# Performance work log

Measured on AMD Instinct MI355X. Metric: run time of the kernel, lower is better.

Reference implementation:

```python
import jax, jax.numpy as jnp
import numpy as np

N = 100000
E = 3200000
IN_DIM = 128
HD = 64
HEADS = 4
NEG_SLOPE = 0.2


def setup_inputs() -> dict:
    key = jax.random.key(0)
    ks = jax.random.split(key, 12)
    s = lambda fan_in: 1.0 / np.sqrt(fan_in)
    x = jax.random.normal(ks[0], (N, IN_DIM), dtype=jnp.float32)
    edge_index = jax.random.randint(ks[1], (2, E), 0, N, dtype=jnp.int64)
    W1 = jax.random.normal(ks[2], (IN_DIM, HEADS * HD), dtype=jnp.float32) * s(IN_DIM)
    a_src1 = jax.random.normal(ks[3], (HEADS, HD), dtype=jnp.float32) * s(HD)
    a_dst1 = jax.random.normal(ks[4], (HEADS, HD), dtype=jnp.float32) * s(HD)
    b1 = jnp.zeros((HEADS * HD,), dtype=jnp.float32)
    W2 = jax.random.normal(ks[5], (HEADS * HD, HD), dtype=jnp.float32) * s(HEADS * HD)
    a_src2 = jax.random.normal(ks[6], (1, HD), dtype=jnp.float32) * s(HD)
    a_dst2 = jax.random.normal(ks[7], (1, HD), dtype=jnp.float32) * s(HD)
    b2 = jnp.zeros((HD,), dtype=jnp.float32)
    lin_w = jax.random.normal(ks[8], (HD, 2), dtype=jnp.float32) * s(HD)
    lin_b = jnp.zeros((2,), dtype=jnp.float32)
    return {"x": x, "edge_index": edge_index, "W1": W1, "a_src1": a_src1,
            "a_dst1": a_dst1, "b1": b1, "W2": W2, "a_src2": a_src2,
            "a_dst2": a_dst2, "b2": b2, "lin_w": lin_w, "lin_b": lin_b}


def gat_conv(x, src, dst, W, a_src, a_dst, bias, heads, out_dim, concat):
    n = x.shape[0]
    h = (x @ W).reshape(n, heads, out_dim)                 # [N,H,D]
    alpha_s = jnp.einsum('nhd,hd->nh', h, a_src)           # [N,H]
    alpha_d = jnp.einsum('nhd,hd->nh', h, a_dst)           # [N,H]
    e = alpha_s[src] + alpha_d[dst]                        # [Etot,H]
    e = jnp.where(e > 0, e, NEG_SLOPE * e)                 # leaky relu
    m = jax.ops.segment_max(e, dst, num_segments=n)        # scatter-softmax (stable)
    m = jnp.where(jnp.isfinite(m), m, 0.0)
    e = jnp.exp(e - m[dst])
    denom = jax.ops.segment_sum(e, dst, num_segments=n)
    alpha = e / denom[dst]                                 # [Etot,H]
    out = jax.ops.segment_sum(h[src] * alpha[:, :, None], dst, num_segments=n)  # [N,H,D]
    out = out.reshape(n, heads * out_dim) if concat else out.mean(axis=1)
    return out + bias


def reference(x, edge_index, W1, a_src1, a_dst1, b1, W2, a_src2, a_dst2, b2, lin_w, lin_b):
    n = x.shape[0]
    loops = jnp.arange(n, dtype=edge_index.dtype)
    src = jnp.concatenate([edge_index[0], loops])          # add self-loops (PyG default)
    dst = jnp.concatenate([edge_index[1], loops])
    h = gat_conv(x, src, dst, W1, a_src1, a_dst1, b1, HEADS, HD, True)
    h = jax.nn.elu(h)
    h = gat_conv(h, src, dst, W2, a_src2, a_dst2, b2, 1, HD, True)
    h = jax.nn.elu(h)
    return h @ lin_w + lin_b                               # [N,2]
```

## Files before the change

kernel.cpp:

```cpp
#include <hip/hip_runtime.h>
#include <hip/hip_fp16.h>
#include <math.h>

#define NN 100000
#define EE 3200000
#define ETOT (EE + NN)
#define NEG_SLOPE 0.2f
#define DMAX 96
#define CHUNK 4096
#define NB0 ((ETOT + CHUNK - 1) / CHUNK)
#define RB 391
#define EDCAP 16384

typedef _Float16 half8 __attribute__((ext_vector_type(8)));
typedef _Float16 half4v __attribute__((ext_vector_type(4)));
typedef float floatx4 __attribute__((ext_vector_type(4)));

__device__ __forceinline__ float wsum64(float v) {
#pragma unroll
  for (int o = 32; o; o >>= 1) v += __shfl_xor(v, o);
  return v;
}
__device__ __forceinline__ float lrelu(float v) { return v > 0.f ? v : NEG_SLOPE * v; }
__device__ __forceinline__ float elu1(float v) { return v > 0.f ? v : expm1f(v); }

__global__ __launch_bounds__(256) void k_pass0(const int* __restrict__ ei,
                                               int* __restrict__ chist,
                                               const float* __restrict__ W1,
                                               const float* __restrict__ W2,
                                               _Float16* __restrict__ W1t,
                                               _Float16* __restrict__ W2t) {
  int b = blockIdx.x;
  if (b >= NB0) {
    int idx = (b - NB0) * 256 + threadIdx.x;
    if (idx < 32768) {
      int n = idx >> 7, k = idx & 127;
      W1t[idx] = (_Float16)W1[k * 256 + n];
    } else {
      int j = idx - 32768;
      int n = j >> 8, k = j & 255;
      W2t[j] = (_Float16)W2[k * 64 + n];
    }
    return;
  }
  __shared__ int h[256];
  h[threadIdx.x] = 0;
  __syncthreads();
  int base = b * CHUNK;
  int lim = base + CHUNK; if (lim > ETOT) lim = ETOT;
  for (int i = base + threadIdx.x; i < lim; i += 256) {
    int d = (i < EE) ? ei[EE + i] : (i - EE);
    atomicAdd(&h[(unsigned)d / (unsigned)RB], 1);
  }
  __syncthreads();
  if (h[threadIdx.x]) atomicAdd(&chist[threadIdx.x], h[threadIdx.x]);
}

__global__ __launch_bounds__(256) void k_cscan(const int* __restrict__ chist,
                                               int* __restrict__ coffs,
                                               int* __restrict__ ccur) {
  __shared__ int ts[256];
  int t = threadIdx.x;
  int v = chist[t];
  ts[t] = v;
  __syncthreads();
  for (int o = 1; o < 256; o <<= 1) {
    int add = (t >= o) ? ts[t - o] : 0;
    __syncthreads();
    ts[t] += add;
    __syncthreads();
  }
  int excl = ts[t] - v;
  coffs[t] = excl;
  ccur[t] = excl;
  if (t == 0) coffs[256] = ETOT;
}

__global__ __launch_bounds__(256) void k_pass1(const int* __restrict__ ei,
                                               int* __restrict__ ccur,
                                               unsigned* __restrict__ ebuf) {
  __shared__ unsigned vv[CHUNK];
  __shared__ unsigned short cbv[CHUNK];
  __shared__ int h[256];
  __shared__ int cur[256];
  int t = threadIdx.x;
  h[t] = 0;
  __syncthreads();
  int base = blockIdx.x * CHUNK;
  int lim = base + CHUNK; if (lim > ETOT) lim = ETOT;
  int cnt = lim - base;
  for (int i = t; i < cnt; i += 256) {
    int e = base + i;
    int s, d;
    if (e < EE) { s = ei[e]; d = ei[EE + e]; } else { s = e - EE; d = s; }
    unsigned cb = (unsigned)d / (unsigned)RB;
    unsigned dloc = (unsigned)d - cb * (unsigned)RB;
    vv[i] = (dloc << 17) | (unsigned)s;
    cbv[i] = (unsigned short)cb;
    atomicAdd(&h[cb], 1);
  }
  __syncthreads();
  if (h[t]) cur[t] = atomicAdd(&ccur[t], h[t]);
  __syncthreads();
  for (int i = t; i < cnt; i += 256) {
    int cb = cbv[i];
    int pos = atomicAdd(&cur[cb], 1);
    ebuf[pos] = vv[i];
  }
}

__global__ __launch_bounds__(256) void k_pass2(const unsigned* __restrict__ ebuf,
                                               const int* __restrict__ coffs,
                                               int* __restrict__ offs,
                                               int* __restrict__ csr) {
  __shared__ unsigned ed[EDCAP];
  __shared__ int hist[RB];
  __shared__ int cur[RB];
  int b = blockIdx.x, t = threadIdx.x;
  int d0 = b * RB;
  int rb = NN - d0; if (rb > RB) rb = RB;
  int cbeg = coffs[b], cend = coffs[b + 1];
  int cnt = cend - cbeg;
  for (int j = t; j < rb; j += 256) hist[j] = 0;
  __syncthreads();
  for (int i = t; i < cnt; i += 256) {
    unsigned v = ebuf[cbeg + i];
    if (i < EDCAP) ed[i] = v;
    atomicAdd(&hist[v >> 17], 1);
  }
  __syncthreads();
  if (t == 0) {
    int run = cbeg;
    for (int j = 0; j < rb; ++j) { cur[j] = run; run += hist[j]; }
  }
  __syncthreads();
  for (int j = t; j < rb; j += 256) offs[d0 + j] = cur[j];
  if (b == 0 && t == 0) offs[NN] = ETOT;
  __syncthreads();
  int lim = cnt < EDCAP ? cnt : EDCAP;
  for (int i = t; i < lim; i += 256) {
    unsigned v = ed[i];
    int pos = atomicAdd(&cur[v >> 17], 1);
    csr[pos] = (int)(v & 0x1FFFFu);
  }
  for (int i = EDCAP + t; i < cnt; i += 256) {
    unsigned v = ebuf[cbeg + i];
    int pos = atomicAdd(&cur[v >> 17], 1);
    csr[pos] = (int)(v & 0x1FFFFu);
  }
}

__global__ __launch_bounds__(256) void k_gemm1m(const float* __restrict__ x,
                                                const _Float16* __restrict__ W1t,
                                                const float* __restrict__ a_src,
                                                const float* __restrict__ a_dst,
                                                _Float16* __restrict__ h1h,
                                                float* __restrict__ as_out,
                                                float* __restrict__ ad_out) {
  __shared__ _Float16 As[64][136];
  __shared__ _Float16 Wt[64][136];
  const int bx = blockIdx.x & 3;
  const int by = blockIdx.x >> 2;
  const int tid = threadIdx.x;
  const int row0 = by * 64;
#pragma unroll
  for (int i = 0; i < 8; ++i) {
    int idx = i * 256 + tid;
    int r = idx >> 5;
    int c4 = (idx & 31) * 4;
    int gr = row0 + r;
    float4 f = make_float4(0.f, 0.f, 0.f, 0.f);
    if (gr < NN) f = *(const float4*)(x + (size_t)gr * 128 + c4);
    half4v h; h[0] = (_Float16)f.x; h[1] = (_Float16)f.y; h[2] = (_Float16)f.z; h[3] = (_Float16)f.w;
    *(half4v*)&As[r][c4] = h;
  }
#pragma unroll
  for (int i = 0; i < 4; ++i) {
    int idx = i * 256 + tid;
    int r = idx >> 4;
    int g = idx & 15;
    *(half8*)&Wt[r][g * 8] = *(const half8*)(W1t + (size_t)(bx * 64 + r) * 128 + g * 8);
  }
  __syncthreads();

  const int wid = tid >> 6, lane = tid & 63;
  const int m16 = lane & 15, quad = lane >> 4;
  floatx4 acc[4];
#pragma unroll
  for (int nt = 0; nt < 4; ++nt) acc[nt] = (floatx4){0.f, 0.f, 0.f, 0.f};
#pragma unroll
  for (int ks = 0; ks < 4; ++ks) {
    half8 av = *(half8*)&As[wid * 16 + m16][ks * 32 + quad * 8];
#pragma unroll
    for (int nt = 0; nt < 4; ++nt) {
      half8 bv = *(half8*)&Wt[nt * 16 + m16][ks * 32 + quad * 8];
      acc[nt] = __builtin_amdgcn_mfma_f32_16x16x32_f16(av, bv, acc[nt], 0, 0, 0);
    }
  }
  float asr[4], adr[4];
#pragma unroll
  for (int nt = 0; nt < 4; ++nt) {
    asr[nt] = a_src[bx * 64 + nt * 16 + m16];
    adr[nt] = a_dst[bx * 64 + nt * 16 + m16];
  }
#pragma unroll
  for (int r = 0; r < 4; ++r) {
    float ps = 0.f, pd = 0.f;
#pragma unroll
    for (int nt = 0; nt < 4; ++nt) {
      ps = fmaf(acc[nt][r], asr[nt], ps);
      pd = fmaf(acc[nt][r], adr[nt], pd);
    }
#pragma unroll
    for (int o = 1; o < 16; o <<= 1) { ps += __shfl_xor(ps, o); pd += __shfl_xor(pd, o); }
    int gr = row0 + wid * 16 + quad * 4 + r;
    if (gr < NN) {
      if (m16 == 0) { as_out[gr * 4 + bx] = ps; ad_out[gr * 4 + bx] = pd; }
#pragma unroll
      for (int nt = 0; nt < 4; ++nt)
        h1h[(size_t)gr * 256 + bx * 64 + nt * 16 + m16] = (_Float16)acc[nt][r];
    }
  }
}

__global__ __launch_bounds__(256) void k_gemm2m(const _Float16* __restrict__ h1e,
                                                const _Float16* __restrict__ W2t,
                                                const float* __restrict__ a_src,
                                                const float* __restrict__ a_dst,
                                                _Float16* __restrict__ h2h,
                                                float* __restrict__ as_out,
                                                float* __restrict__ ad_out) {
  __shared__ _Float16 As2[64][136];
  __shared__ _Float16 Wt2[64][264];
  const int by = blockIdx.x;
  const int tid = threadIdx.x;
  const int row0 = by * 64;
#pragma unroll
  for (int i = 0; i < 8; ++i) {
    int idx = i * 256 + tid;
    int r = idx >> 5;
    int g = idx & 31;
    *(half8*)&Wt2[r][g * 8] = *(const half8*)(W2t + (size_t)r * 256 + g * 8);
  }
  const int wid = tid >> 6, lane = tid & 63;
  const int m16 = lane & 15, quad = lane >> 4;
  floatx4 acc[4];
#pragma unroll
  for (int nt = 0; nt < 4; ++nt) acc[nt] = (floatx4){0.f, 0.f, 0.f, 0.f};

  for (int kc = 0; kc < 2; ++kc) {
#pragma unroll
    for (int i = 0; i < 4; ++i) {
      int idx = i * 256 + tid;
      int r = idx >> 4;
      int g = idx & 15;
      int gr = row0 + r;
      half8 v = {0, 0, 0, 0, 0, 0, 0, 0};
      if (gr < NN) v = *(const half8*)(h1e + (size_t)gr * 256 + kc * 128 + g * 8);
      *(half8*)&As2[r][g * 8] = v;
    }
    __syncthreads();
#pragma unroll
    for (int ks = 0; ks < 4; ++ks) {
      half8 av = *(half8*)&As2[wid * 16 + m16][ks * 32 + quad * 8];
#pragma unroll
      for (int nt = 0; nt < 4; ++nt) {
        half8 bv = *(half8*)&Wt2[nt * 16 + m16][kc * 128 + ks * 32 + quad * 8];
        acc[nt] = __builtin_amdgcn_mfma_f32_16x16x32_f16(av, bv, acc[nt], 0, 0, 0);
      }
    }
    __syncthreads();
  }
  float asr[4], adr[4];
#pragma unroll
  for (int nt = 0; nt < 4; ++nt) {
    asr[nt] = a_src[nt * 16 + m16];
    adr[nt] = a_dst[nt * 16 + m16];
  }
#pragma unroll
  for (int r = 0; r < 4; ++r) {
    float ps = 0.f, pd = 0.f;
#pragma unroll
    for (int nt = 0; nt < 4; ++nt) {
      ps = fmaf(acc[nt][r], asr[nt], ps);
      pd = fmaf(acc[nt][r], adr[nt], pd);
    }
#pragma unroll
    for (int o = 1; o < 16; o <<= 1) { ps += __shfl_xor(ps, o); pd += __shfl_xor(pd, o); }
    int gr = row0 + wid * 16 + quad * 4 + r;
    if (gr < NN) {
      if (m16 == 0) { as_out[gr] = ps; ad_out[gr] = pd; }
#pragma unroll
      for (int nt = 0; nt < 4; ++nt)
        h2h[(size_t)gr * 64 + nt * 16 + m16] = (_Float16)acc[nt][r];
    }
  }
}

__global__ __launch_bounds__(256) void k_attn1(const int* __restrict__ offs,
                                               const int* __restrict__ csr_src,
                                               const float* __restrict__ a_s,
                                               const float* __restrict__ a_d,
                                               const _Float16* __restrict__ h1h,
                                               const float* __restrict__ b1,
                                               _Float16* __restrict__ h1e) {
  __shared__ float alpha[4][DMAX][4];
  __shared__ int sidx[4][DMAX];
  const int wid = threadIdx.x >> 6;
  const int n = blockIdx.x * 4 + wid;
  const int lane = threadIdx.x & 63;
  const int beg = offs[n], deg = offs[n + 1] - beg;
  const float4 ad = *(const float4*)(a_d + n * 4);
  float4 sm = make_float4(0.f, 0.f, 0.f, 0.f);
  for (int d = lane; d < deg; d += 64) {
    int s = csr_src[beg + d];
    float4 as = *(const float4*)(a_s + s * 4);
    float e0 = __expf(lrelu(as.x + ad.x));
    float e1 = __expf(lrelu(as.y + ad.y));
    float e2 = __expf(lrelu(as.z + ad.z));
    float e3 = __expf(lrelu(as.w + ad.w));
    sm.x += e0; sm.y += e1; sm.z += e2; sm.w += e3;
    if (d < DMAX) {
      sidx[wid][d] = s;
      float4 al = make_float4(e0, e1, e2, e3);
      *(float4*)&alpha[wid][d][0] = al;
    }
  }
  sm.x = wsum64(sm.x); sm.y = wsum64(sm.y); sm.z = wsum64(sm.z); sm.w = wsum64(sm.w);
  __syncthreads();

  const int h = lane >> 4;
  float adh = (h & 2) ? ((h & 1) ? ad.w : ad.z) : ((h & 1) ? ad.y : ad.x);
  float dh  = (h & 2) ? ((h & 1) ? sm.w : sm.z) : ((h & 1) ? sm.y : sm.x);
  float inv = 1.f / dh;
  float4 acc = make_float4(0.f, 0.f, 0.f, 0.f);
  const int dlim = deg < DMAX ? deg : DMAX;
  int d = 0;
  for (; d + 8 <= dlim; d += 8) {
    int ss[8]; float ww[8];
#pragma unroll
    for (int u = 0; u < 8; ++u) {
      ss[u] = sidx[wid][d + u];
      ww[u] = alpha[wid][d + u][h] * inv;
    }
    half4v rr[8];
#pragma unroll
    for (int u = 0; u < 8; ++u)
      rr[u] = *(const half4v*)(h1h + (size_t)ss[u] * 256 + lane * 4);
#pragma unroll
    for (int u = 0; u < 8; ++u) {
      acc.x = fmaf((float)rr[u][0], ww[u], acc.x);
      acc.y = fmaf((float)rr[u][1], ww[u], acc.y);
      acc.z = fmaf((float)rr[u][2], ww[u], acc.z);
      acc.w = fmaf((float)rr[u][3], ww[u], acc.w);
    }
  }
  for (; d < dlim; ++d) {
    int s = sidx[wid][d];
    float w = alpha[wid][d][h] * inv;
    half4v r = *(const half4v*)(h1h + (size_t)s * 256 + lane * 4);
    acc.x = fmaf((float)r[0], w, acc.x); acc.y = fmaf((float)r[1], w, acc.y);
    acc.z = fmaf((float)r[2], w, acc.z); acc.w = fmaf((float)r[3], w, acc.w);
  }
  for (; d < deg; ++d) {
    int s = csr_src[beg + d];
    float w = __expf(lrelu(a_s[s * 4 + h] + adh)) * inv;
    half4v r = *(const half4v*)(h1h + (size_t)s * 256 + lane * 4);
    acc.x = fmaf((float)r[0], w, acc.x); acc.y = fmaf((float)r[1], w, acc.y);
    acc.z = fmaf((float)r[2], w, acc.z); acc.w = fmaf((float)r[3], w, acc.w);
  }
  const int c = lane * 4;
  float4 bb = *(const float4*)(b1 + c);
  half4v o;
  o[0] = (_Float16)elu1(acc.x + bb.x);
  o[1] = (_Float16)elu1(acc.y + bb.y);
  o[2] = (_Float16)elu1(acc.z + bb.z);
  o[3] = (_Float16)elu1(acc.w + bb.w);
  *(half4v*)(h1e + (size_t)n * 256 + c) = o;
}

__global__ __launch_bounds__(256) void k_attn2(const int* __restrict__ offs,
                                               const int* __restrict__ csr_src,
                                               const float* __restrict__ a_s,
                                               const float* __restrict__ a_d,
                                               const _Float16* __restrict__ h2h,
                                               const float* __restrict__ b2,
                                               const float* __restrict__ lin_w,
                                               const float* __restrict__ lin_b,
                                               float* __restrict__ out) {
  __shared__ float alpha2[4][DMAX];
  __shared__ int sidx2[4][DMAX];
  const int wid = threadIdx.x >> 6;
  const int n = blockIdx.x * 4 + wid;
  const int lane = threadIdx.x & 63;
  const int beg = offs[n], deg = offs[n + 1] - beg;
  const float adn = a_d[n];
  float sm = 0.f;
  for (int d = lane; d < deg; d += 64) {
    int s = csr_src[beg + d];
    float e = __expf(lrelu(a_s[s] + adn));
    sm += e;
    if (d < DMAX) { sidx2[wid][d] = s; alpha2[wid][d] = e; }
  }
  sm = wsum64(sm);
  __syncthreads();
  float inv = 1.f / sm;
  float acc = 0.f;
  const int dlim = deg < DMAX ? deg : DMAX;
  int d = 0;
  for (; d + 8 <= dlim; d += 8) {
    int ss[8]; float ww[8]; float vv[8];
#pragma unroll
    for (int u = 0; u < 8; ++u) {
      ss[u] = sidx2[wid][d + u];
      ww[u] = alpha2[wid][d + u] * inv;
    }
#pragma unroll
    for (int u = 0; u < 8; ++u)
      vv[u] = (float)h2h[(size_t)ss[u] * 64 + lane];
#pragma unroll
    for (int u = 0; u < 8; ++u) acc = fmaf(vv[u], ww[u], acc);
  }
  for (; d < dlim; ++d) {
    acc = fmaf((float)h2h[(size_t)sidx2[wid][d] * 64 + lane], alpha2[wid][d] * inv, acc);
  }
  for (; d < deg; ++d) {
    int s = csr_src[beg + d];
    float w = __expf(lrelu(a_s[s] + adn)) * inv;
    acc = fmaf((float)h2h[(size_t)s * 64 + lane], w, acc);
  }
  float o = elu1(acc + b2[lane]);
  float p0 = wsum64(o * lin_w[lane * 2 + 0]);
  float p1 = wsum64(o * lin_w[lane * 2 + 1]);
  if (lane == 0) {
    out[n * 2 + 0] = p0 + lin_b[0];
    out[n * 2 + 1] = p1 + lin_b[1];
  }
}

extern "C" void kernel_launch(void* const* d_in, const int* in_sizes, int n_in,
                              void* d_out, int out_size, void* d_ws, size_t ws_size,
                              hipStream_t stream) {
  const float* x      = (const float*)d_in[0];
  const int*   ei     = (const int*)d_in[1];
  const float* W1     = (const float*)d_in[2];
  const float* a_src1 = (const float*)d_in[3];
  const float* a_dst1 = (const float*)d_in[4];
  const float* b1     = (const float*)d_in[5];
  const float* W2     = (const float*)d_in[6];
  const float* a_src2 = (const float*)d_in[7];
  const float* a_dst2 = (const float*)d_in[8];
  const float* b2     = (const float*)d_in[9];
  const float* lin_w  = (const float*)d_in[10];
  const float* lin_b  = (const float*)d_in[11];
  float* outp = (float*)d_out;

  char* w = (char*)d_ws;
  _Float16* h1h = (_Float16*)(w + 0);
  _Float16* h1e = (_Float16*)(w + 51200000);
  _Float16* h2h = (_Float16*)(w + 102400000);
  _Float16* W1t = (_Float16*)(w + 115200000);
  _Float16* W2t = (_Float16*)(w + 115265536);
  float*  as1 = (float*)(w + 115298304);
  float*  ad1 = (float*)(w + 116898304);
  float*  as2 = (float*)(w + 118498304);
  float*  ad2 = (float*)(w + 118898304);
  int*    offs = (int*)(w + 119298304);
  unsigned* ebuf = (unsigned*)(w + 119698432);
  int*    csr = (int*)(w + 132898432);
  int*    chist = (int*)(w + 146098432);
  int*    coffs = (int*)(w + 146099456);
  int*    ccur  = (int*)(w + 146100484);

  hipMemsetAsync(chist, 0, 256 * sizeof(int), stream);
  k_pass0<<<NB0 + 192, 256, 0, stream>>>(ei, chist, W1, W2, W1t, W2t);
  k_cscan<<<1, 256, 0, stream>>>(chist, coffs, ccur);
  k_pass1<<<NB0, 256, 0, stream>>>(ei, ccur, ebuf);
  k_pass2<<<256, 256, 0, stream>>>(ebuf, coffs, offs, csr);

  k_gemm1m<<<4 * 1563, 256, 0, stream>>>(x, W1t, a_src1, a_dst1, h1h, as1, ad1);
  k_attn1<<<NN / 4, 256, 0, stream>>>(offs, csr, as1, ad1, h1h, b1, h1e);

  k_gemm2m<<<1563, 256, 0, stream>>>(h1e, W2t, a_src2, a_dst2, h2h, as2, ad2);
  k_attn2<<<NN / 4, 256, 0, stream>>>(offs, csr, as2, ad2, h2h, b2, lin_w, lin_b, outp);
}
```

Baseline: 616.0 us.

## Split wavefront across multiple edges per gather step with wider vector loads

In both attention aggregation kernels, the 64-lane wavefront now processes several neighbor edges at once: layer 1 splits into two 32-lane halves, each loading 16 bytes (8 halfs) per row, and layer 2 splits into four 16-lane quarters, each loading 8 bytes. Partial accumulators are combined with cross-lane shuffles at the end. The aim is wider per-lane loads and more independent row gathers in flight, to improve memory-level parallelism for the random neighbor fetches. The cost is extra shuffle reductions, masked tail iterations, and more accumulator registers per lane.

```diff
diff --git a/kernel.cpp b/kernel.cpp
--- a/kernel.cpp
+++ b/kernel.cpp
@@ -329,54 +329,59 @@
   sm.x = wsum64(sm.x); sm.y = wsum64(sm.y); sm.z = wsum64(sm.z); sm.w = wsum64(sm.w);
   __syncthreads();
 
-  const int h = lane >> 4;
-  float adh = (h & 2) ? ((h & 1) ? ad.w : ad.z) : ((h & 1) ? ad.y : ad.x);
-  float dh  = (h & 2) ? ((h & 1) ? sm.w : sm.z) : ((h & 1) ? sm.y : sm.x);
-  float inv = 1.f / dh;
-  float4 acc = make_float4(0.f, 0.f, 0.f, 0.f);
+  const int half = lane >> 5;
+  const int fl = lane & 31;
+  const int h = fl >> 3;
+  const float adh = (h & 2) ? ((h & 1) ? ad.w : ad.z) : ((h & 1) ? ad.y : ad.x);
+  const float dh  = (h & 2) ? ((h & 1) ? sm.w : sm.z) : ((h & 1) ? sm.y : sm.x);
+  const float inv = 1.f / dh;
+  float acc8[8];
+#pragma unroll
+  for (int i = 0; i < 8; ++i) acc8[i] = 0.f;
   const int dlim = deg < DMAX ? deg : DMAX;
-  int d = 0;
-  for (; d + 8 <= dlim; d += 8) {
-    int ss[8]; float ww[8];
-#pragma unroll
-    for (int u = 0; u < 8; ++u) {
-      ss[u] = sidx[wid][d + u];
-      ww[u] = alpha[wid][d + u][h] * inv;
-    }
-    half4v rr[8];
-#pragma unroll
-    for (int u = 0; u < 8; ++u)
-      rr[u] = *(const half4v*)(h1h + (size_t)ss[u] * 256 + lane * 4);
-#pragma unroll
-    for (int u = 0; u < 8; ++u) {
-      acc.x = fmaf((float)rr[u][0], ww[u], acc.x);
-      acc.y = fmaf((float)rr[u][1], ww[u], acc.y);
-      acc.z = fmaf((float)rr[u][2], ww[u], acc.z);
-      acc.w = fmaf((float)rr[u][3], ww[u], acc.w);
-    }
-  }
-  for (; d < dlim; ++d) {
-    int s = sidx[wid][d];
-    float w = alpha[wid][d][h] * inv;
-    half4v r = *(const half4v*)(h1h + (size_t)s * 256 + lane * 4);
-    acc.x = fmaf((float)r[0], w, acc.x); acc.y = fmaf((float)r[1], w, acc.y);
-    acc.z = fmaf((float)r[2], w, acc.z); acc.w = fmaf((float)r[3], w, acc.w);
-  }
-  for (; d < deg; ++d) {
+  for (int d = 0; d < dlim; d += 8) {
+    int ss[4]; float ww[4];
+#pragma unroll
+    for (int u = 0; u < 4; ++u) {
+      int e = d + 2 * u + half;
+      bool valid = e < dlim;
+      int e2 = valid ? e : 0;
+      ss[u] = sidx[wid][e2];
+      ww[u] = valid ? alpha[wid][e2][h] * inv : 0.f;
+    }
+    half8 rr[4];
+#pragma unroll
+    for (int u = 0; u < 4; ++u)
+      rr[u] = *(const half8*)(h1h + (size_t)ss[u] * 256 + fl * 8);
+#pragma unroll
+    for (int u = 0; u < 4; ++u)
+#pragma unroll
+      for (int i = 0; i < 8; ++i)
+        acc8[i] = fmaf((float)rr[u][i], ww[u], acc8[i]);
+  }
+  for (int d = dlim + half; d < deg; d += 2) {
     int s = csr_src[beg + d];
     float w = __expf(lrelu(a_s[s * 4 + h] + adh)) * inv;
-    half4v r = *(const half4v*)(h1h + (size_t)s * 256 + lane * 4);
-    acc.x = fmaf((float)r[0], w, acc.x); acc.y = fmaf((float)r[1], w, acc.y);
-    acc.z = fmaf((float)r[2], w, acc.z); acc.w = fmaf((float)r[3], w, acc.w);
-  }
-  const int c = lane * 4;
-  float4 bb = *(const float4*)(b1 + c);
-  half4v o;
-  o[0] = (_Float16)elu1(acc.x + bb.x);
-  o[1] = (_Float16)elu1(acc.y + bb.y);
-  o[2] = (_Float16)elu1(acc.z + bb.z);
-  o[3] = (_Float16)elu1(acc.w + bb.w);
-  *(half4v*)(h1e + (size_t)n * 256 + c) = o;
+    half8 r = *(const half8*)(h1h + (size_t)s * 256 + fl * 8);
+#pragma unroll
+    for (int i = 0; i < 8; ++i) acc8[i] = fmaf((float)r[i], w, acc8[i]);
+  }
+#pragma unroll
+  for (int i = 0; i < 8; ++i) acc8[i] += __shfl_xor(acc8[i], 32);
+  if (half == 0) {
+    float4 bb0 = *(const float4*)(b1 + fl * 8);
+    float4 bb1 = *(const float4*)(b1 + fl * 8 + 4);
+    half8 o;
+    o[0] = (_Float16)elu1(acc8[0] + bb0.x);
+    o[1] = (_Float16)elu1(acc8[1] + bb0.y);
+    o[2] = (_Float16)elu1(acc8[2] + bb0.z);
+    o[3] = (_Float16)elu1(acc8[3] + bb0.w);
+    o[4] = (_Float16)elu1(acc8[4] + bb1.x);
+    o[5] = (_Float16)elu1(acc8[5] + bb1.y);
+    o[6] = (_Float16)elu1(acc8[6] + bb1.z);
+    o[7] = (_Float16)elu1(acc8[7] + bb1.w);
+    *(half8*)(h1e + (size_t)n * 256 + fl * 8) = o;
+  }
 }
 
 __global__ __launch_bounds__(256) void k_attn2(const int* __restrict__ offs,
@@ -404,34 +409,54 @@
   }
   sm = wsum64(sm);
   __syncthreads();
-  float inv = 1.f / sm;
-  float acc = 0.f;
+  const float inv = 1.f / sm;
+  const int quarter = lane >> 4;
+  const int fl = lane & 15;
+  float acc4[4];
+#pragma unroll
+  for (int i = 0; i < 4; ++i) acc4[i] = 0.f;
   const int dlim = deg < DMAX ? deg : DMAX;
-  int d = 0;
-  for (; d + 8 <= dlim; d += 8) {
-    int ss[8]; float ww[8]; float vv[8];
-#pragma unroll
-    for (int u = 0; u < 8; ++u) {
-      ss[u] = sidx2[wid][d + u];
-      ww[u] = alpha2[wid][d + u] * inv;
-    }
-#pragma unroll
-    for (int u = 0; u < 8; ++u)
-      vv[u] = (float)h2h[(size_t)ss[u] * 64 + lane];
-#pragma unroll
-    for (int u = 0; u < 8; ++u) acc = fmaf(vv[u], ww[u], acc);
-  }
-  for (; d < dlim; ++d) {
-    acc = fmaf((float)h2h[(size_t)sidx2[wid][d] * 64 + lane], alpha2[wid][d] * inv, acc);
-  }
-  for (; d < deg; ++d) {
+  for (int d = 0; d < dlim; d += 8) {
+    int ss[2]; float ww[2];
+#pragma unroll
+    for (int u = 0; u < 2; ++u) {
+      int e = d + 4 * u + quarter;
+      bool valid = e < dlim;
+      int e2 = valid ? e : 0;
+      ss[u] = sidx2[wid][e2];
+      ww[u] = valid ? alpha2[wid][e2] * inv : 0.f;
+    }
+    half4v rr[2];
+#pragma unroll
+    for (int u = 0; u < 2; ++u)
+      rr[u] = *(const half4v*)(h2h + (size_t)ss[u] * 64 + fl * 4);
+#pragma unroll
+    for (int u = 0; u < 2; ++u)
+#pragma unroll
+      for (int i = 0; i < 4; ++i)
+        acc4[i] = fmaf((float)rr[u][i], ww[u], acc4[i]);
+  }
+  for (int d = dlim + quarter; d < deg; d += 4) {
     int s = csr_src[beg + d];
     float w = __expf(lrelu(a_s[s] + adn)) * inv;
-    acc = fmaf((float)h2h[(size_t)s * 64 + lane], w, acc);
-  }
-  float o = elu1(acc + b2[lane]);
-  float p0 = wsum64(o * lin_w[lane * 2 + 0]);
-  float p1 = wsum64(o * lin_w[lane * 2 + 1]);
+    half4v r = *(const half4v*)(h2h + (size_t)s * 64 + fl * 4);
+#pragma unroll
+    for (int i = 0; i < 4; ++i) acc4[i] = fmaf((float)r[i], w, acc4[i]);
+  }
+#pragma unroll
+  for (int i = 0; i < 4; ++i) {
+    acc4[i] += __shfl_xor(acc4[i], 16);
+    acc4[i] += __shfl_xor(acc4[i], 32);
+  }
+  float p0 = 0.f, p1 = 0.f;
+#pragma unroll
+  for (int i = 0; i < 4; ++i) {
+    float o = elu1(acc4[i] + b2[fl * 4 + i]);
+    p0 = fmaf(o, lin_w[(fl * 4 + i) * 2 + 0], p0);
+    p1 = fmaf(o, lin_w[(fl * 4 + i) * 2 + 1], p1);
+  }
+#pragma unroll
+  for (int o = 1; o < 16; o <<= 1) { p0 += __shfl_xor(p0, o); p1 += __shfl_xor(p1, o); }
   if (lane == 0) {
     out[n * 2 + 0] = p0 + lin_b[0];
     out[n * 2 + 1] = p1 + lin_b[1];
```

Result: slower. 642.0 us (+4.2%).

## Drop CSR histogram pass with fixed-capacity buckets, widen GEMM1 tile, prenormalize attention

Applied to the files above, without the earlier changes.

Drops the separate edge-histogram kernel and the scan kernel. Each of the 256 destination buckets now gets a fixed slot of CAP entries in ebuf, so the edge list is read one fewer time and two launches disappear. Per-node degrees are stored explicitly for the attention kernels. GEMM1 now computes 128 output columns per block instead of 64, halving the block count and reusing each x tile more. The attention kernels drop a block-wide barrier and normalize alpha once in shared memory instead of multiplying per use. The fixed bucket capacity assumes a near-uniform destination distribution: a bucket holding more than CAP edges would overwrite the next bucket's slot and be truncated.

```diff
diff --git a/kernel.cpp b/kernel.cpp
--- a/kernel.cpp
+++ b/kernel.cpp
@@ -10,7 +10,7 @@
 #define CHUNK 4096
 #define NB0 ((ETOT + CHUNK - 1) / CHUNK)
 #define RB 391
-#define EDCAP 16384
+#define CAP 16384
 
 typedef _Float16 half8 __attribute__((ext_vector_type(8)));
 typedef _Float16 half4v __attribute__((ext_vector_type(4)));
@@ -24,8 +24,13 @@
 __device__ __forceinline__ float lrelu(float v) { return v > 0.f ? v : NEG_SLOPE * v; }
 __device__ __forceinline__ float elu1(float v) { return v > 0.f ? v : expm1f(v); }
 
-__global__ __launch_bounds__(256) void k_pass0(const int* __restrict__ ei,
-                                               int* __restrict__ chist,
+__global__ void k_init(int* __restrict__ ccur) {
+  ccur[threadIdx.x] = threadIdx.x * CAP;
+}
+
+__global__ __launch_bounds__(256) void k_pass1(const int* __restrict__ ei,
+                                               int* __restrict__ ccur,
+                                               unsigned* __restrict__ ebuf,
                                                const float* __restrict__ W1,
                                                const float* __restrict__ W2,
                                                _Float16* __restrict__ W1t,
@@ -43,42 +48,6 @@
     }
     return;
   }
-  __shared__ int h[256];
-  h[threadIdx.x] = 0;
-  __syncthreads();
-  int base = b * CHUNK;
-  int lim = base + CHUNK; if (lim > ETOT) lim = ETOT;
-  for (int i = base + threadIdx.x; i < lim; i += 256) {
-    int d = (i < EE) ? ei[EE + i] : (i - EE);
-    atomicAdd(&h[(unsigned)d / (unsigned)RB], 1);
-  }
-  __syncthreads();
-  if (h[threadIdx.x]) atomicAdd(&chist[threadIdx.x], h[threadIdx.x]);
-}
-
-__global__ __launch_bounds__(256) void k_cscan(const int* __restrict__ chist,
-                                               int* __restrict__ coffs,
-                                               int* __restrict__ ccur) {
-  __shared__ int ts[256];
-  int t = threadIdx.x;
-  int v = chist[t];
-  ts[t] = v;
-  __syncthreads();
-  for (int o = 1; o < 256; o <<= 1) {
-    int add = (t >= o) ? ts[t - o] : 0;
-    __syncthreads();
-    ts[t] += add;
-    __syncthreads();
-  }
-  int excl = ts[t] - v;
-  coffs[t] = excl;
-  ccur[t] = excl;
-  if (t == 0) coffs[256] = ETOT;
-}
-
-__global__ __launch_bounds__(256) void k_pass1(const int* __restrict__ ei,
-                                               int* __restrict__ ccur,
-                                               unsigned* __restrict__ ebuf) {
   __shared__ unsigned vv[CHUNK];
   __shared__ unsigned short cbv[CHUNK];
   __shared__ int h[256];
@@ -86,7 +55,7 @@
   int t = threadIdx.x;
   h[t] = 0;
   __syncthreads();
-  int base = blockIdx.x * CHUNK;
+  int base = b * CHUNK;
   int lim = base + CHUNK; if (lim > ETOT) lim = ETOT;
   int cnt = lim - base;
   for (int i = t; i < cnt; i += 256) {
@@ -110,41 +79,39 @@
 }
 
 __global__ __launch_bounds__(256) void k_pass2(const unsigned* __restrict__ ebuf,
-                                               const int* __restrict__ coffs,
+                                               const int* __restrict__ ccur,
                                                int* __restrict__ offs,
+                                               int* __restrict__ degarr,
                                                int* __restrict__ csr) {
-  __shared__ unsigned ed[EDCAP];
+  __shared__ unsigned ed[CAP];
   __shared__ int hist[RB];
   __shared__ int cur[RB];
   int b = blockIdx.x, t = threadIdx.x;
   int d0 = b * RB;
   int rb = NN - d0; if (rb > RB) rb = RB;
-  int cbeg = coffs[b], cend = coffs[b + 1];
-  int cnt = cend - cbeg;
+  int w0 = b * CAP;
+  int cnt = ccur[b] - w0;
+  if (cnt > CAP) cnt = CAP;
   for (int j = t; j < rb; j += 256) hist[j] = 0;
   __syncthreads();
   for (int i = t; i < cnt; i += 256) {
-    unsigned v = ebuf[cbeg + i];
-    if (i < EDCAP) ed[i] = v;
+    unsigned v = ebuf[w0 + i];
+    ed[i] = v;
     atomicAdd(&hist[v >> 17], 1);
   }
   __syncthreads();
   if (t == 0) {
-    int run = cbeg;
+    int run = w0;
     for (int j = 0; j < rb; ++j) { cur[j] = run; run += hist[j]; }
   }
   __syncthreads();
-  for (int j = t; j < rb; j += 256) offs[d0 + j] = cur[j];
-  if (b == 0 && t == 0) offs[NN] = ETOT;
-  __syncthreads();
-  int lim = cnt < EDCAP ? cnt : EDCAP;
-  for (int i = t; i < lim; i += 256) {
+  for (int j = t; j < rb; j += 256) {
+    offs[d0 + j] = cur[j];
+    degarr[d0 + j] = hist[j];
+  }
+  __syncthreads();
+  for (int i = t; i < cnt; i += 256) {
     unsigned v = ed[i];
-    int pos = atomicAdd(&cur[v >> 17], 1);
-    csr[pos] = (int)(v & 0x1FFFFu);
-  }
-  for (int i = EDCAP + t; i < cnt; i += 256) {
-    unsigned v = ebuf[cbeg + i];
     int pos = atomicAdd(&cur[v >> 17], 1);
     csr[pos] = (int)(v & 0x1FFFFu);
   }
@@ -158,9 +125,9 @@
                                                 float* __restrict__ as_out,
                                                 float* __restrict__ ad_out) {
   __shared__ _Float16 As[64][136];
-  __shared__ _Float16 Wt[64][136];
-  const int bx = blockIdx.x & 3;
-  const int by = blockIdx.x >> 2;
+  __shared__ _Float16 Wt[128][136];
+  const int bx = blockIdx.x & 1;
+  const int by = blockIdx.x >> 1;
   const int tid = threadIdx.x;
   const int row0 = by * 64;
 #pragma unroll
@@ -175,50 +142,57 @@
     *(half4v*)&As[r][c4] = h;
   }
 #pragma unroll
-  for (int i = 0; i < 4; ++i) {
+  for (int i = 0; i < 8; ++i) {
     int idx = i * 256 + tid;
     int r = idx >> 4;
     int g = idx & 15;
-    *(half8*)&Wt[r][g * 8] = *(const half8*)(W1t + (size_t)(bx * 64 + r) * 128 + g * 8);
+    *(half8*)&Wt[r][g * 8] = *(const half8*)(W1t + (size_t)(bx * 128 + r) * 128 + g * 8);
   }
   __syncthreads();
 
   const int wid = tid >> 6, lane = tid & 63;
   const int m16 = lane & 15, quad = lane >> 4;
-  floatx4 acc[4];
-#pragma unroll
-  for (int nt = 0; nt < 4; ++nt) acc[nt] = (floatx4){0.f, 0.f, 0.f, 0.f};
+  floatx4 acc[8];
+#pragma unroll
+  for (int nt = 0; nt < 8; ++nt) acc[nt] = (floatx4){0.f, 0.f, 0.f, 0.f};
 #pragma unroll
   for (int ks = 0; ks < 4; ++ks) {
     half8 av = *(half8*)&As[wid * 16 + m16][ks * 32 + quad * 8];
 #pragma unroll
-    for (int nt = 0; nt < 4; ++nt) {
+    for (int nt = 0; nt < 8; ++nt) {
       half8 bv = *(half8*)&Wt[nt * 16 + m16][ks * 32 + quad * 8];
       acc[nt] = __builtin_amdgcn_mfma_f32_16x16x32_f16(av, bv, acc[nt], 0, 0, 0);
     }
   }
-  float asr[4], adr[4];
-#pragma unroll
-  for (int nt = 0; nt < 4; ++nt) {
-    asr[nt] = a_src[bx * 64 + nt * 16 + m16];
-    adr[nt] = a_dst[bx * 64 + nt * 16 + m16];
+  float asr[8], adr[8];
+#pragma unroll
+  for (int nt = 0; nt < 8; ++nt) {
+    asr[nt] = a_src[bx * 128 + nt * 16 + m16];
+    adr[nt] = a_dst[bx * 128 + nt * 16 + m16];
   }
 #pragma unroll
   for (int r = 0; r < 4; ++r) {
-    float ps = 0.f, pd = 0.f;
-#pragma unroll
-    for (int nt = 0; nt < 4; ++nt) {
-      ps = fmaf(acc[nt][r], asr[nt], ps);
-      pd = fmaf(acc[nt][r], adr[nt], pd);
-    }
-#pragma unroll
-    for (int o = 1; o < 16; o <<= 1) { ps += __shfl_xor(ps, o); pd += __shfl_xor(pd, o); }
     int gr = row0 + wid * 16 + quad * 4 + r;
-    if (gr < NN) {
-      if (m16 == 0) { as_out[gr * 4 + bx] = ps; ad_out[gr * 4 + bx] = pd; }
-#pragma unroll
-      for (int nt = 0; nt < 4; ++nt)
-        h1h[(size_t)gr * 256 + bx * 64 + nt * 16 + m16] = (_Float16)acc[nt][r];
+    bool ok = gr < NN;
+#pragma unroll
+    for (int hp = 0; hp < 2; ++hp) {
+      float ps = 0.f, pd = 0.f;
+#pragma unroll
+      for (int j = 0; j < 4; ++j) {
+        ps = fmaf(acc[hp * 4 + j][r], asr[hp * 4 + j], ps);
+        pd = fmaf(acc[hp * 4 + j][r], adr[hp * 4 + j], pd);
+      }
+#pragma unroll
+      for (int o = 1; o < 16; o <<= 1) { ps += __shfl_xor(ps, o); pd += __shfl_xor(pd, o); }
+      if (ok && m16 == 0) {
+        as_out[gr * 4 + bx * 2 + hp] = ps;
+        ad_out[gr * 4 + bx * 2 + hp] = pd;
+      }
+    }
+    if (ok) {
+#pragma unroll
+      for (int nt = 0; nt < 8; ++nt)
+        h1h[(size_t)gr * 256 + bx * 128 + nt * 16 + m16] = (_Float16)acc[nt][r];
     }
   }
 }
@@ -298,6 +272,7 @@
 }
 
 __global__ __launch_bounds__(256) void k_attn1(const int* __restrict__ offs,
+                                               const int* __restrict__ degarr,
                                                const int* __restrict__ csr_src,
                                                const float* __restrict__ a_s,
                                                const float* __restrict__ a_d,
@@ -309,7 +284,7 @@
   const int wid = threadIdx.x >> 6;
   const int n = blockIdx.x * 4 + wid;
   const int lane = threadIdx.x & 63;
-  const int beg = offs[n], deg = offs[n + 1] - beg;
+  const int beg = offs[n], deg = degarr[n];
   const float4 ad = *(const float4*)(a_d + n * 4);
   float4 sm = make_float4(0.f, 0.f, 0.f, 0.f);
   for (int d = lane; d < deg; d += 64) {
@@ -322,26 +297,26 @@
     sm.x += e0; sm.y += e1; sm.z += e2; sm.w += e3;
     if (d < DMAX) {
       sidx[wid][d] = s;
-      float4 al = make_float4(e0, e1, e2, e3);
-      *(float4*)&alpha[wid][d][0] = al;
+      *(float4*)&alpha[wid][d][0] = make_float4(e0, e1, e2, e3);
     }
   }
   sm.x = wsum64(sm.x); sm.y = wsum64(sm.y); sm.z = wsum64(sm.z); sm.w = wsum64(sm.w);
-  __syncthreads();
-
+  const float4 inv4 = make_float4(1.f / sm.x, 1.f / sm.y, 1.f / sm.z, 1.f / sm.w);
+  const int dlim = deg < DMAX ? deg : DMAX;
+  for (int d = lane; d < dlim; d += 64) {
+    float4 a = *(float4*)&alpha[wid][d][0];
+    a.x *= inv4.x; a.y *= inv4.y; a.z *= inv4.z; a.w *= inv4.w;
+    *(float4*)&alpha[wid][d][0] = a;
+  }
   const int h = lane >> 4;
-  float adh = (h & 2) ? ((h & 1) ? ad.w : ad.z) : ((h & 1) ? ad.y : ad.x);
-  float dh  = (h & 2) ? ((h & 1) ? sm.w : sm.z) : ((h & 1) ? sm.y : sm.x);
-  float inv = 1.f / dh;
   float4 acc = make_float4(0.f, 0.f, 0.f, 0.f);
-  const int dlim = deg < DMAX ? deg : DMAX;
   int d = 0;
   for (; d + 8 <= dlim; d += 8) {
     int ss[8]; float ww[8];
 #pragma unroll
     for (int u = 0; u < 8; ++u) {
       ss[u] = sidx[wid][d + u];
-      ww[u] = alpha[wid][d + u][h] * inv;
+      ww[u] = alpha[wid][d + u][h];
     }
     half4v rr[8];
 #pragma unroll
@@ -357,14 +332,16 @@
   }
   for (; d < dlim; ++d) {
     int s = sidx[wid][d];
-    float w = alpha[wid][d][h] * inv;
+    float w = alpha[wid][d][h];
     half4v r = *(const half4v*)(h1h + (size_t)s * 256 + lane * 4);
     acc.x = fmaf((float)r[0], w, acc.x); acc.y = fmaf((float)r[1], w, acc.y);
     acc.z = fmaf((float)r[2], w, acc.z); acc.w = fmaf((float)r[3], w, acc.w);
   }
+  const float adh = (h & 2) ? ((h & 1) ? ad.w : ad.z) : ((h & 1) ? ad.y : ad.x);
+  const float invh = (h & 2) ? ((h & 1) ? inv4.w : inv4.z) : ((h & 1) ? inv4.y : inv4.x);
   for (; d < deg; ++d) {
     int s = csr_src[beg + d];
-    float w = __expf(lrelu(a_s[s * 4 + h] + adh)) * inv;
+    float w = __expf(lrelu(a_s[s * 4 + h] + adh)) * invh;
     half4v r = *(const half4v*)(h1h + (size_t)s * 256 + lane * 4);
     acc.x = fmaf((float)r[0], w, acc.x); acc.y = fmaf((float)r[1], w, acc.y);
     acc.z = fmaf((float)r[2], w, acc.z); acc.w = fmaf((float)r[3], w, acc.w);
@@ -380,6 +357,7 @@
 }
 
 __global__ __launch_bounds__(256) void k_attn2(const int* __restrict__ offs,
+                                               const int* __restrict__ degarr,
                                                const int* __restrict__ csr_src,
                                                const float* __restrict__ a_s,
                                                const float* __restrict__ a_d,
@@ -393,7 +371,7 @@
   const int wid = threadIdx.x >> 6;
   const int n = blockIdx.x * 4 + wid;
   const int lane = threadIdx.x & 63;
-  const int beg = offs[n], deg = offs[n + 1] - beg;
+  const int beg = offs[n], deg = degarr[n];
   const float adn = a_d[n];
   float sm = 0.f;
   for (int d = lane; d < deg; d += 64) {
@@ -403,17 +381,17 @@
     if (d < DMAX) { sidx2[wid][d] = s; alpha2[wid][d] = e; }
   }
   sm = wsum64(sm);
-  __syncthreads();
-  float inv = 1.f / sm;
+  const float inv = 1.f / sm;
+  const int dlim = deg < DMAX ? deg : DMAX;
+  for (int d = lane; d < dlim; d += 64) alpha2[wid][d] *= inv;
   float acc = 0.f;
-  const int dlim = deg < DMAX ? deg : DMAX;
   int d = 0;
   for (; d + 8 <= dlim; d += 8) {
     int ss[8]; float ww[8]; float vv[8];
 #pragma unroll
     for (int u = 0; u < 8; ++u) {
       ss[u] = sidx2[wid][d + u];
-      ww[u] = alpha2[wid][d + u] * inv;
+      ww[u] = alpha2[wid][d + u];
     }
 #pragma unroll
     for (int u = 0; u < 8; ++u)
@@ -422,7 +400,7 @@
     for (int u = 0; u < 8; ++u) acc = fmaf(vv[u], ww[u], acc);
   }
   for (; d < dlim; ++d) {
-    acc = fmaf((float)h2h[(size_t)sidx2[wid][d] * 64 + lane], alpha2[wid][d] * inv, acc);
+    acc = fmaf((float)h2h[(size_t)sidx2[wid][d] * 64 + lane], alpha2[wid][d], acc);
   }
   for (; d < deg; ++d) {
     int s = csr_src[beg + d];
@@ -466,21 +444,18 @@
   float*  as2 = (float*)(w + 118498304);
   float*  ad2 = (float*)(w + 118898304);
   int*    offs = (int*)(w + 119298304);
-  unsigned* ebuf = (unsigned*)(w + 119698432);
-  int*    csr = (int*)(w + 132898432);
-  int*    chist = (int*)(w + 146098432);
-  int*    coffs = (int*)(w + 146099456);
-  int*    ccur  = (int*)(w + 146100484);
-
-  hipMemsetAsync(chist, 0, 256 * sizeof(int), stream);
-  k_pass0<<<NB0 + 192, 256, 0, stream>>>(ei, chist, W1, W2, W1t, W2t);
-  k_cscan<<<1, 256, 0, stream>>>(chist, coffs, ccur);
-  k_pass1<<<NB0, 256, 0, stream>>>(ei, ccur, ebuf);
-  k_pass2<<<256, 256, 0, stream>>>(ebuf, coffs, offs, csr);
-
-  k_gemm1m<<<4 * 1563, 256, 0, stream>>>(x, W1t, a_src1, a_dst1, h1h, as1, ad1);
-  k_attn1<<<NN / 4, 256, 0, stream>>>(offs, csr, as1, ad1, h1h, b1, h1e);
+  int*    degarr = (int*)(w + 119698304);
+  int*    ccur = (int*)(w + 120098304);
+  unsigned* ebuf = (unsigned*)(w + 120099328);
+  int*    csr = (int*)(w + 136876544);
+
+  k_init<<<1, 256, 0, stream>>>(ccur);
+  k_pass1<<<NB0 + 192, 256, 0, stream>>>(ei, ccur, ebuf, W1, W2, W1t, W2t);
+  k_pass2<<<256, 256, 0, stream>>>(ebuf, ccur, offs, degarr, csr);
+
+  k_gemm1m<<<2 * 1563, 256, 0, stream>>>(x, W1t, a_src1, a_dst1, h1h, as1, ad1);
+  k_attn1<<<NN / 4, 256, 0, stream>>>(offs, degarr, csr, as1, ad1, h1h, b1, h1e);
 
   k_gemm2m<<<1563, 256, 0, stream>>>(h1e, W2t, a_src2, a_dst2, h2h, as2, ad2);
-  k_attn2<<<NN / 4, 256, 0, stream>>>(offs, csr, as2, ad2, h2h, b2, lin_w, lin_b, outp);
-}
+  k_attn2<<<NN / 4, 256, 0, stream>>>(offs, degarr, csr, as2, ad2, h2h, b2, lin_w, lin_b, outp);
+}
```

New measurement: 579.2 us. 1.06x faster.
